# Kernel optimization log

Hardware: AMD Instinct MI355X
Metric: run time of the kernel (lower is better)

The kernel has to match this reference:

```python
import jax, jax.numpy as jnp
import numpy as np

B, L, D = 4, 2048, 256
PH, EH = 64, 256
MAX_DISP = 5.0
MIN_DISP = 0.5
REP = 0.3
POWER = 2.0
SURFACE = 103.0
NROW = 46
OFFSET = 0.1
SPACING = SURFACE / (NROW - 1)
DANGER = SPACING / 4.0


def _gelu(x):
    return jax.nn.gelu(x, approximate=False)  # torch nn.GELU default = exact erf


def setup_inputs() -> dict:
    key = jax.random.key(0)
    ks = jax.random.split(key, 8)

    def lin(k, i, o):
        return jax.random.normal(k, (i, o), jnp.float32) * 0.02, jnp.zeros((o,), jnp.float32)

    pe_w1, pe_b1 = lin(ks[0], 2, PH)
    pe_w2, pe_b2 = lin(ks[1], PH, PH)
    em_w1, em_b1 = lin(ks[2], D + PH, EH)
    em_w2, em_b2 = lin(ks[3], EH, EH // 2)
    em_w3, em_b3 = lin(ks[4], EH // 2, 1)
    ln_g = jnp.ones((EH,), jnp.float32)
    ln_b = jnp.zeros((EH,), jnp.float32)
    latents = jax.random.normal(ks[5], (B, L, D), jnp.float32)
    positions = jax.random.uniform(ks[6], (B, L, 2), jnp.float32) * SURFACE
    return dict(latents=latents, positions=positions,
                pe_w1=pe_w1, pe_b1=pe_b1, pe_w2=pe_w2, pe_b2=pe_b2,
                em_w1=em_w1, em_b1=em_b1, ln_g=ln_g, ln_b=ln_b,
                em_w2=em_w2, em_b2=em_b2, em_w3=em_w3, em_b3=em_b3,
                layer_idx=0)


def _predict_errors(latents, positions, pe_w1, pe_b1, pe_w2, pe_b2,
                    em_w1, em_b1, ln_g, ln_b, em_w2, em_b2, em_w3, em_b3):
    # ErrorPredictor: pos encoder MLP + error MLP with LayerNorm + Softplus
    pf = _gelu(positions @ pe_w1 + pe_b1) @ pe_w2 + pe_b2          # [B,L,PH]
    x = jnp.concatenate([latents, pf], axis=-1)                     # [B,L,D+PH]
    h = x @ em_w1 + em_b1                                           # [B,L,EH]
    mu = h.mean(-1, keepdims=True)
    var = ((h - mu) ** 2).mean(-1, keepdims=True)
    h = (h - mu) / jnp.sqrt(var + 1e-5) * ln_g + ln_b
    h = _gelu(h)
    h = _gelu(h @ em_w2 + em_b2)                                    # [B,L,EH//2]
    return jax.nn.softplus(h @ em_w3 + em_b3)[..., 0]               # [B,L]


def _forward(latents, positions, pe_w1, pe_b1, pe_w2, pe_b2,
             em_w1, em_b1, ln_g, ln_b, em_w2, em_b2, em_w3, em_b3):
    # error prediction on detached inputs
    errors = _predict_errors(jax.lax.stop_gradient(latents), jax.lax.stop_gradient(positions),
                             pe_w1, pe_b1, pe_w2, pe_b2,
                             em_w1, em_b1, ln_g, ln_b, em_w2, em_b2, em_w3, em_b3)
    e_min = errors.min(-1, keepdims=True)
    e_max = errors.max(-1, keepdims=True)
    errors_norm = (errors - e_min) / (e_max - e_min + 1e-8) + OFFSET  # [B,L]

    # all-pairs delta_ij = pos_j - pos_i : [B,L,L,2]
    delta = positions[:, None, :, :] - positions[:, :, None, :]
    dist = jnp.maximum(jnp.sqrt((delta ** 2).sum(-1)), 1e-6)          # [B,L,L]
    direction = delta / dist[..., None]
    mask = ~jnp.eye(L, dtype=bool)                                    # exclude self

    gmag = (errors_norm[:, None, :] / dist ** POWER) * mask           # [B,L,L]
    gravity = (direction * gmag[..., None]).sum(axis=2)               # [B,L,2]

    viol = jnp.maximum(DANGER - dist, 0.0)
    rmag = (jnp.exp(viol / DANGER) - 1.0) * mask
    repulsion = -(direction * rmag[..., None]).sum(axis=2)            # [B,L,2]

    total = gravity + REP * repulsion
    fmag = jnp.sqrt((total ** 2).sum(-1, keepdims=True))              # [B,L,1]
    fdir = total / (fmag + 1e-8)
    fmean = fmag.mean(axis=1, keepdims=True)
    frel = fmag / (fmean + 1e-8)
    dmag = jnp.clip(frel * MAX_DISP, MIN_DISP, MAX_DISP)
    displacement = fdir * dmag
    new_positions = positions + displacement
    return new_positions, displacement, errors


def reference(latents, positions, pe_w1, pe_b1, pe_w2, pe_b2,
              em_w1, em_b1, ln_g, ln_b, em_w2, em_b2, em_w3, em_b3, layer_idx):
    # share_weights=True -> layer_idx selects the same predictor
    return _forward(latents, positions, pe_w1, pe_b1, pe_w2, pe_b2,
                    em_w1, em_b1, ln_g, ln_b, em_w2, em_b2, em_w3, em_b3)
```

## Files before the change

### kernel.cpp

```cpp
#include <hip/hip_runtime.h>
#include <math.h>

#define NB 4
#define NL 2048
#define ND 256
#define PPB 32

__device__ __forceinline__ float gelu_exact(float x) {
    return 0.5f * x * (1.0f + erff(x * 0.70710678118654752f));
}

#define DANGER_F ((float)(103.0 / 45.0 / 4.0))
#define DANGER2_SLACK_F ((float)(103.0 / 45.0 / 4.0 * 103.0 / 45.0 / 4.0 * 1.0001))
#define REP_F 0.3f
#define MAXD_F 5.0f
#define MIND_F 0.5f
#define OFF_F 0.1f

__global__ __launch_bounds__(512) void mlp_kernel(
    const float* __restrict__ latents, const float* __restrict__ positions,
    const float* __restrict__ pe_w1, const float* __restrict__ pe_b1,
    const float* __restrict__ pe_w2, const float* __restrict__ pe_b2,
    const float* __restrict__ em_w1, const float* __restrict__ em_b1,
    const float* __restrict__ ln_g, const float* __restrict__ ln_b,
    const float* __restrict__ em_w2, const float* __restrict__ em_b2,
    const float* __restrict__ em_w3, const float* __restrict__ em_b3,
    float* __restrict__ errors_out)
{
    const int t  = threadIdx.x;
    const int g0 = blockIdx.x * PPB;
    const int l  = t & 63;
    const int p0 = (t >> 6) * 4;

    __shared__ float xs[PPB][320];
    __shared__ float pf1[PPB][64];
    __shared__ float posl[2 * PPB];

    {
        const float4* src = (const float4*)(latents + (size_t)g0 * ND);
        #pragma unroll
        for (int m = 0; m < 4; ++m) {
            const int q = t + 512 * m;
            const float4 v = src[q];
            *(float4*)&xs[q >> 6][(q & 63) * 4] = v;
        }
    }
    if (t < PPB) ((float2*)posl)[t] = ((const float2*)positions)[g0 + t];
    __syncthreads();

    {
        const int p = t >> 4, j0 = t & 15;
        const float px = posl[2 * p], py = posl[2 * p + 1];
        #pragma unroll
        for (int h = 0; h < 4; ++h) {
            const int j = j0 + 16 * h;
            pf1[p][j] = gelu_exact(fmaf(px, pe_w1[j], fmaf(py, pe_w1[64 + j], pe_b1[j])));
        }
    }
    __syncthreads();
    {
        const int p = t >> 4, j0 = t & 15;
        #pragma unroll
        for (int h = 0; h < 4; ++h) {
            const int j = j0 + 16 * h;
            float a = pe_b2[j];
            #pragma unroll 4
            for (int k = 0; k < 64; ++k)
                a = fmaf(pf1[p][k], pe_w2[k * 64 + j], a);
            xs[p][ND + j] = a;
        }
    }
    __syncthreads();

    float acc[4][4];
    {
        const float4 b1 = *(const float4*)&em_b1[4 * l];
        #pragma unroll
        for (int p = 0; p < 4; ++p) {
            acc[p][0] = b1.x; acc[p][1] = b1.y; acc[p][2] = b1.z; acc[p][3] = b1.w;
        }
    }

#define MM_CHUNK(KK, W)                                                          \
    {                                                                            \
        float xk[4][4];                                                          \
        _Pragma("unroll")                                                        \
        for (int p = 0; p < 4; ++p) {                                            \
            const float4 xq = *(const float4*)&xs[p0 + p][(KK)];                 \
            xk[p][0] = xq.x; xk[p][1] = xq.y; xk[p][2] = xq.z; xk[p][3] = xq.w;  \
        }                                                                        \
        _Pragma("unroll")                                                        \
        for (int u = 0; u < 4; ++u) {                                            \
            _Pragma("unroll")                                                    \
            for (int p = 0; p < 4; ++p) {                                        \
                acc[p][0] = fmaf(xk[p][u], W[u].x, acc[p][0]);                   \
                acc[p][1] = fmaf(xk[p][u], W[u].y, acc[p][1]);                   \
                acc[p][2] = fmaf(xk[p][u], W[u].z, acc[p][2]);                   \
                acc[p][3] = fmaf(xk[p][u], W[u].w, acc[p][3]);                   \
            }                                                                    \
        }                                                                        \
    }

    {
        const float4* __restrict__ W1 = (const float4*)em_w1;
        float4 wA[4], wB[4];
        #pragma unroll
        for (int u = 0; u < 4; ++u) wA[u] = W1[(size_t)(0 + u) * 64 + l];
        #pragma unroll
        for (int u = 0; u < 4; ++u) wB[u] = W1[(size_t)(4 + u) * 64 + l];
        for (int k = 0; k < 312; k += 8) {
            MM_CHUNK(k, wA);
            #pragma unroll
            for (int u = 0; u < 4; ++u) wA[u] = W1[(size_t)(k + 8 + u) * 64 + l];
            MM_CHUNK(k + 4, wB);
            #pragma unroll
            for (int u = 0; u < 4; ++u) wB[u] = W1[(size_t)(k + 12 + u) * 64 + l];
        }
        MM_CHUNK(312, wA);
        MM_CHUNK(316, wB);
    }
#undef MM_CHUNK

    float mu[4], rstd[4];
    #pragma unroll
    for (int p = 0; p < 4; ++p) {
        float s = acc[p][0] + acc[p][1] + acc[p][2] + acc[p][3];
        float q = acc[p][0] * acc[p][0] + acc[p][1] * acc[p][1]
                + acc[p][2] * acc[p][2] + acc[p][3] * acc[p][3];
        #pragma unroll
        for (int m = 1; m < 64; m <<= 1) {
            s += __shfl_xor(s, m);
            q += __shfl_xor(q, m);
        }
        mu[p] = s * (1.0f / 256.0f);
        rstd[p] = 1.0f / sqrtf(q * (1.0f / 256.0f) - mu[p] * mu[p] + 1e-5f);
    }

    {
        const float4 g4 = *(const float4*)&ln_g[4 * l];
        const float4 b4 = *(const float4*)&ln_b[4 * l];
        #pragma unroll
        for (int p = 0; p < 4; ++p) {
            float4 o;
            o.x = gelu_exact(fmaf((acc[p][0] - mu[p]) * rstd[p], g4.x, b4.x));
            o.y = gelu_exact(fmaf((acc[p][1] - mu[p]) * rstd[p], g4.y, b4.y));
            o.z = gelu_exact(fmaf((acc[p][2] - mu[p]) * rstd[p], g4.z, b4.z));
            o.w = gelu_exact(fmaf((acc[p][3] - mu[p]) * rstd[p], g4.w, b4.w));
            *(float4*)&xs[p0 + p][4 * l] = o;
        }
    }

    float a2[4][2];
    {
        const float2 b2 = *(const float2*)&em_b2[2 * l];
        #pragma unroll
        for (int p = 0; p < 4; ++p) { a2[p][0] = b2.x; a2[p][1] = b2.y; }
    }

#define H2_CHUNK(KK, W)                                                          \
    {                                                                            \
        float xk[4][4];                                                          \
        _Pragma("unroll")                                                        \
        for (int p = 0; p < 4; ++p) {                                            \
            const float4 xq = *(const float4*)&xs[p0 + p][(KK)];                 \
            xk[p][0] = xq.x; xk[p][1] = xq.y; xk[p][2] = xq.z; xk[p][3] = xq.w;  \
        }                                                                        \
        _Pragma("unroll")                                                        \
        for (int u = 0; u < 4; ++u) {                                            \
            _Pragma("unroll")                                                    \
            for (int p = 0; p < 4; ++p) {                                        \
                a2[p][0] = fmaf(xk[p][u], W[u].x, a2[p][0]);                     \
                a2[p][1] = fmaf(xk[p][u], W[u].y, a2[p][1]);                     \
            }                                                                    \
        }                                                                        \
    }

    {
        const float2* __restrict__ W2 = (const float2*)em_w2;
        float2 wA[4], wB[4];
        #pragma unroll
        for (int u = 0; u < 4; ++u) wA[u] = W2[(size_t)(0 + u) * 64 + l];
        #pragma unroll
        for (int u = 0; u < 4; ++u) wB[u] = W2[(size_t)(4 + u) * 64 + l];
        for (int k = 0; k < 248; k += 8) {
            H2_CHUNK(k, wA);
            #pragma unroll
            for (int u = 0; u < 4; ++u) wA[u] = W2[(size_t)(k + 8 + u) * 64 + l];
            H2_CHUNK(k + 4, wB);
            #pragma unroll
            for (int u = 0; u < 4; ++u) wB[u] = W2[(size_t)(k + 12 + u) * 64 + l];
        }
        H2_CHUNK(248, wA);
        H2_CHUNK(252, wB);
    }
#undef H2_CHUNK

    {
        const float2 w3 = *(const float2*)&em_w3[2 * l];
        float r[4];
        #pragma unroll
        for (int p = 0; p < 4; ++p)
            r[p] = fmaf(gelu_exact(a2[p][0]), w3.x, gelu_exact(a2[p][1]) * w3.y);
        #pragma unroll
        for (int m = 1; m < 64; m <<= 1) {
            #pragma unroll
            for (int p = 0; p < 4; ++p) r[p] += __shfl_xor(r[p], m);
        }
        if (l == 0) {
            #pragma unroll
            for (int p = 0; p < 4; ++p) {
                const float x = r[p] + em_b3[0];
                errors_out[g0 + p0 + p] = fmaxf(x, 0.0f) + log1pf(expf(-fabsf(x)));
            }
        }
    }
}

__global__ __launch_bounds__(256) void minmax_kernel(const float* __restrict__ errors,
                                                     float2* __restrict__ mnden,
                                                     float2* __restrict__ force)
{
    const int b = blockIdx.x, t = threadIdx.x;
    const float* e = errors + b * NL;
    float mn = 1e30f, mx = -1e30f;
    #pragma unroll
    for (int m = 0; m < 8; ++m) {
        const float v = e[t + 256 * m];
        mn = fminf(mn, v); mx = fmaxf(mx, v);
    }
    #pragma unroll
    for (int m = 1; m < 64; m <<= 1) {
        mn = fminf(mn, __shfl_xor(mn, m));
        mx = fmaxf(mx, __shfl_xor(mx, m));
    }
    __shared__ float rmn[4], rmx[4];
    const int lane = t & 63, wid = t >> 6;
    if (lane == 0) { rmn[wid] = mn; rmx[wid] = mx; }
    __syncthreads();
    if (t == 0) {
        mn = fminf(fminf(rmn[0], rmn[1]), fminf(rmn[2], rmn[3]));
        mx = fmaxf(fmaxf(rmx[0], rmx[1]), fmaxf(rmx[2], rmx[3]));
        mnden[b] = make_float2(mn, (mx - mn) + 1e-8f);
    }
    #pragma unroll
    for (int m = 0; m < 8; ++m)
        force[b * NL + t + 256 * m] = make_float2(0.0f, 0.0f);
}

__global__ __launch_bounds__(256) void pair_kernel(
    const float* __restrict__ positions, const float* __restrict__ errors,
    const float2* __restrict__ mnden, float2* __restrict__ force)
{
    const int t = threadIdx.x;
    int bid = blockIdx.x;
    const int jc = bid & 31; bid >>= 5;
    const int ic = bid & 7;  bid >>= 3;
    const int b  = bid;
    const int i  = ic * 256 + t;

    const float2 pi = ((const float2*)positions)[b * NL + i];

    __shared__ float4 pj4[64];
    if (t < 64) {
        const int j = jc * 64 + t;
        const float2 pj = ((const float2*)positions)[b * NL + j];
        const float2 md = mnden[b];
        pj4[t] = make_float4(pj.x, pj.y, (errors[b * NL + j] - md.x) / md.y + OFF_F, 0.0f);
    }
    __syncthreads();

    float tx = 0.f, ty = 0.f;
    #pragma unroll 4
    for (int m = 0; m < 64; ++m) {
        const float4 v = pj4[m];
        const float dx = v.x - pi.x;
        const float dy = v.y - pi.y;
        const float r2 = fmaf(dx, dx, dy * dy);
        const bool tiny = (r2 < 1e-12f);
        const float invd = tiny ? 1e6f : rsqrtf(r2);
        float w = v.z * invd * invd;
        if (r2 < DANGER2_SLACK_F) {
            const float dist = fmaxf(sqrtf(r2), 1e-6f);
            const float viol = DANGER_F - dist;
            if (viol > 0.f)
                w -= REP_F * (expf(viol / DANGER_F) - 1.0f);
        }
        const float g = w * invd;
        tx = fmaf(dx, g, tx);
        ty = fmaf(dy, g, ty);
    }
    atomicAdd(&force[b * NL + i].x, tx);
    atomicAdd(&force[b * NL + i].y, ty);
}

__global__ __launch_bounds__(512) void final_kernel(
    const float* __restrict__ positions, const float2* __restrict__ force,
    float* __restrict__ out)
{
    const int b = blockIdx.x, t = threadIdx.x;
    float tx[4], ty[4], fm[4];
    float fsum = 0.f;
    #pragma unroll
    for (int m = 0; m < 4; ++m) {
        const int i = t + 512 * m;
        const float2 v = force[b * NL + i];
        tx[m] = v.x; ty[m] = v.y;
        fm[m] = sqrtf(fmaf(v.x, v.x, v.y * v.y));
        fsum += fm[m];
    }
    #pragma unroll
    for (int m = 1; m < 64; m <<= 1) fsum += __shfl_xor(fsum, m);
    __shared__ float rs[8];
    const int lane = t & 63, wid = t >> 6;
    if (lane == 0) rs[wid] = fsum;
    __syncthreads();
    float fmean = 0.f;
    #pragma unroll
    for (int w = 0; w < 8; ++w) fmean += rs[w];
    fmean *= (1.0f / NL);

    float* newpos = out;
    float* disp   = out + 2 * NB * NL;
    #pragma unroll
    for (int m = 0; m < 4; ++m) {
        const int i = t + 512 * m;
        const float fmag = fm[m];
        const float frel = fmag / (fmean + 1e-8f);
        const float dmag = fminf(fmaxf(frel * MAXD_F, MIND_F), MAXD_F);
        const float fdx = tx[m] / (fmag + 1e-8f);
        const float fdy = ty[m] / (fmag + 1e-8f);
        const float dpx = fdx * dmag, dpy = fdy * dmag;
        const float2 pi = ((const float2*)positions)[b * NL + i];
        ((float2*)newpos)[b * NL + i] = make_float2(pi.x + dpx, pi.y + dpy);
        ((float2*)disp)[b * NL + i]   = make_float2(dpx, dpy);
    }
}

extern "C" void kernel_launch(void* const* d_in, const int* in_sizes, int n_in,
                              void* d_out, int out_size, void* d_ws, size_t ws_size,
                              hipStream_t stream)
{
    const float* latents   = (const float*)d_in[0];
    const float* positions = (const float*)d_in[1];
    const float* pe_w1 = (const float*)d_in[2];
    const float* pe_b1 = (const float*)d_in[3];
    const float* pe_w2 = (const float*)d_in[4];
    const float* pe_b2 = (const float*)d_in[5];
    const float* em_w1 = (const float*)d_in[6];
    const float* em_b1 = (const float*)d_in[7];
    const float* ln_g  = (const float*)d_in[8];
    const float* ln_b  = (const float*)d_in[9];
    const float* em_w2 = (const float*)d_in[10];
    const float* em_b2 = (const float*)d_in[11];
    const float* em_w3 = (const float*)d_in[12];
    const float* em_b3 = (const float*)d_in[13];

    float* out = (float*)d_out;
    float* errors = out + 2 * 2 * NB * NL;

    float2* mnden = (float2*)d_ws;
    float2* force = mnden + NB;

    mlp_kernel<<<NB * NL / PPB, 512, 0, stream>>>(
        latents, positions, pe_w1, pe_b1, pe_w2, pe_b2,
        em_w1, em_b1, ln_g, ln_b, em_w2, em_b2, em_w3, em_b3, errors);

    minmax_kernel<<<NB, 256, 0, stream>>>(errors, mnden, force);

    pair_kernel<<<NB * 8 * 32, 256, 0, stream>>>(positions, errors, mnden, force);

    final_kernel<<<NB, 512, 0, stream>>>(positions, force, out);
}
```

Measured before the change: 163.2 us.

## Stage MLP weights through double-buffered LDS and fuse minmax into pair kernel

The MLP kernel now loads em_w1 and em_w2 tiles cooperatively into a double-buffered shared-memory buffer, so the whole block shares each tile instead of every wave streaming weights from global memory per thread. This adds about 32 KB of LDS and a barrier per tile. The separate minmax kernel is removed: each pair block recomputes the per-batch min/max redundantly, and the force-buffer zeroing moves into the MLP kernel. That saves one launch at the cost of repeated reduction work in 1024 blocks. pf1 padding also changes to 68.

```diff
diff --git a/kernel.cpp b/kernel.cpp
--- a/kernel.cpp
+++ b/kernel.cpp
@@ -25,7 +25,7 @@
     const float* __restrict__ ln_g, const float* __restrict__ ln_b,
     const float* __restrict__ em_w2, const float* __restrict__ em_b2,
     const float* __restrict__ em_w3, const float* __restrict__ em_b3,
-    float* __restrict__ errors_out)
+    float* __restrict__ errors_out, float2* __restrict__ force)
 {
     const int t  = threadIdx.x;
     const int g0 = blockIdx.x * PPB;
@@ -33,8 +33,11 @@
     const int p0 = (t >> 6) * 4;
 
     __shared__ float xs[PPB][320];
-    __shared__ float pf1[PPB][64];
+    __shared__ float pf1[PPB][68];
     __shared__ float posl[2 * PPB];
+    __shared__ float wb[2][16 * 256];
+
+    if (t < 32) force[blockIdx.x * 32 + t] = make_float2(0.0f, 0.0f);
 
     {
         const float4* src = (const float4*)(latents + (size_t)g0 * ND);
@@ -80,46 +83,42 @@
             acc[p][0] = b1.x; acc[p][1] = b1.y; acc[p][2] = b1.z; acc[p][3] = b1.w;
         }
     }
-
-#define MM_CHUNK(KK, W)                                                          \
-    {                                                                            \
-        float xk[4][4];                                                          \
-        _Pragma("unroll")                                                        \
-        for (int p = 0; p < 4; ++p) {                                            \
-            const float4 xq = *(const float4*)&xs[p0 + p][(KK)];                 \
-            xk[p][0] = xq.x; xk[p][1] = xq.y; xk[p][2] = xq.z; xk[p][3] = xq.w;  \
-        }                                                                        \
-        _Pragma("unroll")                                                        \
-        for (int u = 0; u < 4; ++u) {                                            \
-            _Pragma("unroll")                                                    \
-            for (int p = 0; p < 4; ++p) {                                        \
-                acc[p][0] = fmaf(xk[p][u], W[u].x, acc[p][0]);                   \
-                acc[p][1] = fmaf(xk[p][u], W[u].y, acc[p][1]);                   \
-                acc[p][2] = fmaf(xk[p][u], W[u].z, acc[p][2]);                   \
-                acc[p][3] = fmaf(xk[p][u], W[u].w, acc[p][3]);                   \
-            }                                                                    \
-        }                                                                        \
-    }
-
-    {
-        const float4* __restrict__ W1 = (const float4*)em_w1;
-        float4 wA[4], wB[4];
-        #pragma unroll
-        for (int u = 0; u < 4; ++u) wA[u] = W1[(size_t)(0 + u) * 64 + l];
-        #pragma unroll
-        for (int u = 0; u < 4; ++u) wB[u] = W1[(size_t)(4 + u) * 64 + l];
-        for (int k = 0; k < 312; k += 8) {
-            MM_CHUNK(k, wA);
+    {
+        const float4* __restrict__ W1v = (const float4*)em_w1;
+        float4 r0 = W1v[t];
+        float4 r1 = W1v[t + 512];
+        for (int kt = 0; kt < 20; ++kt) {
+            float* dst = wb[kt & 1];
+            *(float4*)&dst[t * 4]         = r0;
+            *(float4*)&dst[(t + 512) * 4] = r1;
+            if (kt < 19) {
+                r0 = W1v[(kt + 1) * 1024 + t];
+                r1 = W1v[(kt + 1) * 1024 + t + 512];
+            }
+            __syncthreads();
+            const float* wcur = wb[kt & 1];
             #pragma unroll
-            for (int u = 0; u < 4; ++u) wA[u] = W1[(size_t)(k + 8 + u) * 64 + l];
-            MM_CHUNK(k + 4, wB);
-            #pragma unroll
-            for (int u = 0; u < 4; ++u) wB[u] = W1[(size_t)(k + 12 + u) * 64 + l];
-        }
-        MM_CHUNK(312, wA);
-        MM_CHUNK(316, wB);
-    }
-#undef MM_CHUNK
+            for (int kk = 0; kk < 16; kk += 4) {
+                float xk[4][4];
+                #pragma unroll
+                for (int p = 0; p < 4; ++p) {
+                    const float4 xq = *(const float4*)&xs[p0 + p][kt * 16 + kk];
+                    xk[p][0] = xq.x; xk[p][1] = xq.y; xk[p][2] = xq.z; xk[p][3] = xq.w;
+                }
+                #pragma unroll
+                for (int u = 0; u < 4; ++u) {
+                    const float4 w = *(const float4*)&wcur[(kk + u) * 256 + 4 * l];
+                    #pragma unroll
+                    for (int p = 0; p < 4; ++p) {
+                        acc[p][0] = fmaf(xk[p][u], w.x, acc[p][0]);
+                        acc[p][1] = fmaf(xk[p][u], w.y, acc[p][1]);
+                        acc[p][2] = fmaf(xk[p][u], w.z, acc[p][2]);
+                        acc[p][3] = fmaf(xk[p][u], w.w, acc[p][3]);
+                    }
+                }
+            }
+        }
+    }
 
     float mu[4], rstd[4];
     #pragma unroll
@@ -135,7 +134,6 @@
         mu[p] = s * (1.0f / 256.0f);
         rstd[p] = 1.0f / sqrtf(q * (1.0f / 256.0f) - mu[p] * mu[p] + 1e-5f);
     }
-
     {
         const float4 g4 = *(const float4*)&ln_g[4 * l];
         const float4 b4 = *(const float4*)&ln_b[4 * l];
@@ -156,44 +154,35 @@
         #pragma unroll
         for (int p = 0; p < 4; ++p) { a2[p][0] = b2.x; a2[p][1] = b2.y; }
     }
-
-#define H2_CHUNK(KK, W)                                                          \
-    {                                                                            \
-        float xk[4][4];                                                          \
-        _Pragma("unroll")                                                        \
-        for (int p = 0; p < 4; ++p) {                                            \
-            const float4 xq = *(const float4*)&xs[p0 + p][(KK)];                 \
-            xk[p][0] = xq.x; xk[p][1] = xq.y; xk[p][2] = xq.z; xk[p][3] = xq.w;  \
-        }                                                                        \
-        _Pragma("unroll")                                                        \
-        for (int u = 0; u < 4; ++u) {                                            \
-            _Pragma("unroll")                                                    \
-            for (int p = 0; p < 4; ++p) {                                        \
-                a2[p][0] = fmaf(xk[p][u], W[u].x, a2[p][0]);                     \
-                a2[p][1] = fmaf(xk[p][u], W[u].y, a2[p][1]);                     \
-            }                                                                    \
-        }                                                                        \
-    }
-
-    {
-        const float2* __restrict__ W2 = (const float2*)em_w2;
-        float2 wA[4], wB[4];
-        #pragma unroll
-        for (int u = 0; u < 4; ++u) wA[u] = W2[(size_t)(0 + u) * 64 + l];
-        #pragma unroll
-        for (int u = 0; u < 4; ++u) wB[u] = W2[(size_t)(4 + u) * 64 + l];
-        for (int k = 0; k < 248; k += 8) {
-            H2_CHUNK(k, wA);
+    {
+        const float4* __restrict__ W2v = (const float4*)em_w2;
+        float4 s = W2v[t];
+        for (int kt = 0; kt < 16; ++kt) {
+            float* dst = wb[kt & 1];
+            *(float4*)&dst[t * 4] = s;
+            if (kt < 15) s = W2v[(kt + 1) * 512 + t];
+            __syncthreads();
+            const float* wcur = wb[kt & 1];
             #pragma unroll
-            for (int u = 0; u < 4; ++u) wA[u] = W2[(size_t)(k + 8 + u) * 64 + l];
-            H2_CHUNK(k + 4, wB);
-            #pragma unroll
-            for (int u = 0; u < 4; ++u) wB[u] = W2[(size_t)(k + 12 + u) * 64 + l];
-        }
-        H2_CHUNK(248, wA);
-        H2_CHUNK(252, wB);
-    }
-#undef H2_CHUNK
+            for (int kk = 0; kk < 16; kk += 4) {
+                float xk[4][4];
+                #pragma unroll
+                for (int p = 0; p < 4; ++p) {
+                    const float4 xq = *(const float4*)&xs[p0 + p][kt * 16 + kk];
+                    xk[p][0] = xq.x; xk[p][1] = xq.y; xk[p][2] = xq.z; xk[p][3] = xq.w;
+                }
+                #pragma unroll
+                for (int u = 0; u < 4; ++u) {
+                    const float2 w = *(const float2*)&wcur[(kk + u) * 128 + 2 * l];
+                    #pragma unroll
+                    for (int p = 0; p < 4; ++p) {
+                        a2[p][0] = fmaf(xk[p][u], w.x, a2[p][0]);
+                        a2[p][1] = fmaf(xk[p][u], w.y, a2[p][1]);
+                    }
+                }
+            }
+        }
+    }
 
     {
         const float2 w3 = *(const float2*)&em_w3[2 * l];
@@ -216,11 +205,17 @@
     }
 }
 
-__global__ __launch_bounds__(256) void minmax_kernel(const float* __restrict__ errors,
-                                                     float2* __restrict__ mnden,
-                                                     float2* __restrict__ force)
+__global__ __launch_bounds__(256) void pair_kernel(
+    const float* __restrict__ positions, const float* __restrict__ errors,
+    float2* __restrict__ force)
 {
-    const int b = blockIdx.x, t = threadIdx.x;
+    const int t = threadIdx.x;
+    int bid = blockIdx.x;
+    const int jc = bid & 31;
+    const int ic = (bid >> 5) & 7;
+    const int b  = bid >> 8;
+    const int i  = ic * 256 + t;
+
     const float* e = errors + b * NL;
     float mn = 1e30f, mx = -1e30f;
     #pragma unroll
@@ -237,26 +232,9 @@
     const int lane = t & 63, wid = t >> 6;
     if (lane == 0) { rmn[wid] = mn; rmx[wid] = mx; }
     __syncthreads();
-    if (t == 0) {
-        mn = fminf(fminf(rmn[0], rmn[1]), fminf(rmn[2], rmn[3]));
-        mx = fmaxf(fmaxf(rmx[0], rmx[1]), fmaxf(rmx[2], rmx[3]));
-        mnden[b] = make_float2(mn, (mx - mn) + 1e-8f);
-    }
-    #pragma unroll
-    for (int m = 0; m < 8; ++m)
-        force[b * NL + t + 256 * m] = make_float2(0.0f, 0.0f);
-}
-
-__global__ __launch_bounds__(256) void pair_kernel(
-    const float* __restrict__ positions, const float* __restrict__ errors,
-    const float2* __restrict__ mnden, float2* __restrict__ force)
-{
-    const int t = threadIdx.x;
-    int bid = blockIdx.x;
-    const int jc = bid & 31; bid >>= 5;
-    const int ic = bid & 7;  bid >>= 3;
-    const int b  = bid;
-    const int i  = ic * 256 + t;
+    mn = fminf(fminf(rmn[0], rmn[1]), fminf(rmn[2], rmn[3]));
+    mx = fmaxf(fmaxf(rmx[0], rmx[1]), fmaxf(rmx[2], rmx[3]));
+    const float den = (mx - mn) + 1e-8f;
 
     const float2 pi = ((const float2*)positions)[b * NL + i];
 
@@ -264,8 +242,7 @@
     if (t < 64) {
         const int j = jc * 64 + t;
         const float2 pj = ((const float2*)positions)[b * NL + j];
-        const float2 md = mnden[b];
-        pj4[t] = make_float4(pj.x, pj.y, (errors[b * NL + j] - md.x) / md.y + OFF_F, 0.0f);
+        pj4[t] = make_float4(pj.x, pj.y, (e[j] - mn) / den + OFF_F, 0.0f);
     }
     __syncthreads();
 
@@ -358,16 +335,13 @@
     float* out = (float*)d_out;
     float* errors = out + 2 * 2 * NB * NL;
 
-    float2* mnden = (float2*)d_ws;
-    float2* force = mnden + NB;
+    float2* force = (float2*)d_ws;
 
     mlp_kernel<<<NB * NL / PPB, 512, 0, stream>>>(
         latents, positions, pe_w1, pe_b1, pe_w2, pe_b2,
-        em_w1, em_b1, ln_g, ln_b, em_w2, em_b2, em_w3, em_b3, errors);
-
-    minmax_kernel<<<NB, 256, 0, stream>>>(errors, mnden, force);
-
-    pair_kernel<<<NB * 8 * 32, 256, 0, stream>>>(positions, errors, mnden, force);
+        em_w1, em_b1, ln_g, ln_b, em_w2, em_b2, em_w3, em_b3, errors, force);
+
+    pair_kernel<<<NB * 8 * 32, 256, 0, stream>>>(positions, errors, force);
 
     final_kernel<<<NB, 512, 0, stream>>>(positions, force, out);
 }
```

Measured after the change: 157.2 us. -3.6%, faster.
